# Performance work log

Hardware: AMD Instinct MI355X
Metric: run time of the kernel (lower is better)

Reference implementation:

```python
import jax, jax.numpy as jnp
import numpy as np

N, IN_DIM, H, ATT_DIM, OUT_DIM = 4096, 512, 8, 64, 64
ATT_BIAS = 0.5


def setup_inputs() -> dict:
    key = jax.random.key(0)
    ks = jax.random.split(key, 12)
    s_in = 1.0 / np.sqrt(IN_DIM)
    s_o = 1.0 / np.sqrt(H * OUT_DIM)
    return {
        "Q": jax.random.normal(ks[0], (N, IN_DIM), jnp.float32),
        "K": jax.random.normal(ks[1], (N, IN_DIM), jnp.float32),
        "V": jax.random.normal(ks[2], (N, IN_DIM), jnp.float32),
        "adj": jax.random.uniform(ks[3], (N, N), jnp.float32),
        "WQ": jax.random.normal(ks[4], (IN_DIM, H * ATT_DIM), jnp.float32) * s_in,
        "bQ": jnp.zeros((H * ATT_DIM,), jnp.float32),
        "WK": jax.random.normal(ks[5], (IN_DIM, H * ATT_DIM), jnp.float32) * s_in,
        "bK": jnp.zeros((H * ATT_DIM,), jnp.float32),
        "WV": jax.random.normal(ks[6], (IN_DIM, H * OUT_DIM), jnp.float32) * s_in,
        "bV": jnp.zeros((H * OUT_DIM,), jnp.float32),
        "WO": jax.random.normal(ks[7], (H * OUT_DIM, OUT_DIM), jnp.float32) * s_o,
        "bO": jnp.zeros((OUT_DIM,), jnp.float32),
    }


def reference(Q, K, V, adj, WQ, bQ, WK, bK, WV, bV, WO, bO):
    scale = ATT_DIM ** -0.5
    q = (Q @ WQ + bQ).reshape(N, H, ATT_DIM)   # [N,H,d]
    k = (K @ WK + bK).reshape(N, H, ATT_DIM)   # [N,H,d]
    v = (V @ WV + bV).reshape(N, H, OUT_DIM)   # [N,H,e]
    # scaled QK^T per head: [H,N,N]
    scores = jnp.einsum("nhd,mhd->hnm", q * scale, k)
    # sigmoid -> bias subtract -> +0.1*adj -> softmax over keys
    scores = jax.nn.sigmoid(scores) - ATT_BIAS + 0.1 * adj[None, :, :]
    attn = jax.nn.softmax(scores, axis=2)
    # attend values (dropout p=0 => identity), concat heads, project
    out = jnp.einsum("hnm,mhe->nhe", attn, v).reshape(N, H * OUT_DIM)
    return out @ WO + bO
```

## Files before the change

kernel.cpp:

```cpp
#include <hip/hip_runtime.h>
#include <hip/hip_bf16.h>

#define N_TOK  4096
#define HD     512
#define NH     8
#define NSPLIT 2

typedef short v8s __attribute__((ext_vector_type(8)));
typedef float v4f __attribute__((ext_vector_type(4)));
typedef unsigned short u16;

#define QSCALE   0.18033688011112042f
#define ADJ2     0.14426950408889634f
#define EA0 0.999410f
#define EA1 1.016220f
#define EA2 0.423120f
#define EA3 0.279120f

__device__ __forceinline__ float bf2f(u16 x) {
  union { unsigned int u; float f; } c; c.u = ((unsigned int)x) << 16; return c.f;
}
__device__ __forceinline__ u16 f2bf(float f) {
  union { float f; unsigned int u; } c; c.f = f;
  return (u16)((c.u + 0x7fffu + ((c.u >> 16) & 1u)) >> 16);
}
__device__ __forceinline__ float fast_exp2(float x) {
#if __has_builtin(__builtin_amdgcn_exp2f)
  return __builtin_amdgcn_exp2f(x);
#else
  return exp2f(x);
#endif
}
__device__ __forceinline__ unsigned int pk_bf16(float a, float b) {
  union { __hip_bfloat162 h; unsigned int u; } c;
  c.h = __float22bfloat162_rn(make_float2(a, b));
  return c.u;
}

__device__ __forceinline__ bool detect_f32(const u16* __restrict__ q) {
  int l = threadIdx.x & 63;
  u16 e = q[2 * l];
  float x = bf2f(e);
  int ex = (e >> 7) & 0xFF;
  float ax = fabsf(x);
  bool ok = (ex != 0xFF) && (ax < 64.f) && (ax > 1e-30f);
  unsigned long long m = __ballot(ok);
  return __popcll(m) < 48;
}
__device__ __forceinline__ float bias_ld(const void* b, int i, bool f32) {
  return f32 ? ((const float*)b)[i] : bf2f(((const u16*)b)[i]);
}

__global__ __launch_bounds__(256) void conv_adjE_k(const void* __restrict__ adj, u16* __restrict__ adjE,
                                                   const u16* __restrict__ Qdet) {
  bool f32 = detect_f32(Qdet);
  int i = blockIdx.x * 256 + threadIdx.x;
  float4 f;
  if (f32) {
    f = ((const float4*)adj)[i];
  } else {
    short4 v = ((const short4*)adj)[i];
    f.x = bf2f((u16)v.x); f.y = bf2f((u16)v.y); f.z = bf2f((u16)v.z); f.w = bf2f((u16)v.w);
  }
  unsigned int d0 = pk_bf16(fast_exp2(f.x * ADJ2), fast_exp2(f.y * ADJ2));
  unsigned int d1 = pk_bf16(fast_exp2(f.z * ADJ2), fast_exp2(f.w * ADJ2));
  ((uint2*)adjE)[i] = make_uint2(d0, d1);
}

__global__ __launch_bounds__(256) void tr_w_k(const void* W0, const void* W1, const void* W2, const void* W3,
                                              u16* t0, u16* t1, u16* t2, u16* t3,
                                              const u16* __restrict__ Qdet) {
  bool f32 = detect_f32(Qdet);
  int z = blockIdx.z;
  const void* in; u16* out; int C;
  if (z == 0)      { in = W0; out = t0; C = 512; }
  else if (z == 1) { in = W1; out = t1; C = 512; }
  else if (z == 2) { in = W2; out = t2; C = 512; }
  else             { in = W3; out = t3; C = 64; if (blockIdx.y) return; }
  const int R = 512;
  __shared__ __align__(16) u16 tile[64][72];
  const int r0 = blockIdx.x * 64, c0 = blockIdx.y * 64;
  const int t = threadIdx.x;
#pragma unroll
  for (int rep = 0; rep < 2; ++rep) {
    int idx = (t + rep * 256) * 8;
    int r = idx >> 6, c = idx & 63;
    if (f32) {
      const float* sp = (const float*)in + (size_t)(r0 + r) * C + (c0 + c);
      float4 a = *(const float4*)sp, b = *(const float4*)(sp + 4);
      uint4 q = make_uint4(pk_bf16(a.x, a.y), pk_bf16(a.z, a.w),
                           pk_bf16(b.x, b.y), pk_bf16(b.z, b.w));
      *(uint4*)&tile[r][c] = q;
    } else {
      *(v8s*)&tile[r][c] = *(const v8s*)((const u16*)in + (size_t)(r0 + r) * C + (c0 + c));
    }
  }
  __syncthreads();
#pragma unroll
  for (int rep = 0; rep < 2; ++rep) {
    int idx = (t + rep * 256) * 8;
    int oc = idx >> 6, orr = idx & 63;
    u16 tmp[8];
#pragma unroll
    for (int j = 0; j < 8; ++j) tmp[j] = tile[orr + j][oc];
    *(v8s*)(out + (size_t)(c0 + oc) * R + (r0 + orr)) = *(v8s*)tmp;
  }
}

__global__ __launch_bounds__(256) void gemm_qkv_k(const void* A0, const void* A1, const void* A2,
                                                  const u16* __restrict__ t0, const u16* __restrict__ t1,
                                                  const u16* __restrict__ t2,
                                                  const void* b0, const void* b1, const void* b2,
                                                  u16* __restrict__ qb, u16* __restrict__ kb,
                                                  u16* __restrict__ vtb) {
  __shared__ __align__(16) u16 As[64][72];
  __shared__ __align__(16) u16 Bs[64][72];
  bool f32 = detect_f32((const u16*)A0);
  int z = blockIdx.z;
  const void* Araw = (z == 0) ? A0 : (z == 1) ? A1 : A2;
  const u16* Bt    = (z == 0) ? t0 : (z == 1) ? t1 : t2;
  const void* bias = (z == 0) ? b0 : (z == 1) ? b1 : b2;
  const bool vt = (z == 2);
  const int i0 = blockIdx.x * 64, j0 = blockIdx.y * 64;
  const int t = threadIdx.x, w = t >> 6, l = t & 63, quad = l >> 4, l15 = l & 15;
  v4f acc[4] = {};
  for (int k0 = 0; k0 < 512; k0 += 64) {
#pragma unroll
    for (int rep = 0; rep < 2; ++rep) {
      int idx = (t + rep * 256) * 8;
      int r = idx >> 6, c = idx & 63;
      if (f32) {
        const float* sp = (const float*)Araw + (size_t)(i0 + r) * 512 + k0 + c;
        float4 fa = *(const float4*)sp, fb = *(const float4*)(sp + 4);
        uint4 q = make_uint4(pk_bf16(fa.x, fa.y), pk_bf16(fa.z, fa.w),
                             pk_bf16(fb.x, fb.y), pk_bf16(fb.z, fb.w));
        *(uint4*)&As[r][c] = q;
      } else {
        *(v8s*)&As[r][c] = *(const v8s*)((const u16*)Araw + (size_t)(i0 + r) * 512 + k0 + c);
      }
      *(v8s*)&Bs[r][c] = *(const v8s*)(Bt + (size_t)(j0 + r) * 512 + k0 + c);
    }
    __syncthreads();
    if (vt) {
#pragma unroll
      for (int h = 0; h < 2; ++h) {
        v8s a = *(const v8s*)&As[w * 16 + l15][h * 32 + quad * 8];
#pragma unroll
        for (int cb = 0; cb < 4; ++cb) {
          v8s b = *(const v8s*)&Bs[cb * 16 + l15][h * 32 + quad * 8];
          acc[cb] = __builtin_amdgcn_mfma_f32_16x16x32_bf16(b, a, acc[cb], 0, 0, 0);
        }
      }
    } else {
#pragma unroll
      for (int h = 0; h < 2; ++h) {
        v8s a = *(const v8s*)&As[w * 16 + l15][h * 32 + quad * 8];
#pragma unroll
        for (int cb = 0; cb < 4; ++cb) {
          v8s b = *(const v8s*)&Bs[cb * 16 + l15][h * 32 + quad * 8];
          acc[cb] = __builtin_amdgcn_mfma_f32_16x16x32_bf16(a, b, acc[cb], 0, 0, 0);
        }
      }
    }
    __syncthreads();
  }
  if (vt) {
#pragma unroll
    for (int cb = 0; cb < 4; ++cb) {
#pragma unroll
      for (int r = 0; r < 4; ++r) {
        int jj = j0 + cb * 16 + quad * 4 + r;
        int ii = i0 + w * 16 + l15;
        vtb[(size_t)jj * N_TOK + ii] = f2bf(acc[cb][r] + bias_ld(bias, jj, f32));
      }
    }
  } else {
    const float oscale = (z == 0) ? QSCALE : 1.0f;
    u16* C = (z == 0) ? qb : kb;
#pragma unroll
    for (int cb = 0; cb < 4; ++cb) {
      int col = j0 + cb * 16 + l15;
      float bv = bias_ld(bias, col, f32);
#pragma unroll
      for (int r = 0; r < 4; ++r) {
        int row = i0 + w * 16 + quad * 4 + r;
        C[(size_t)row * HD + col] = f2bf((acc[cb][r] + bv) * oscale);
      }
    }
  }
}

__global__ __launch_bounds__(256, 4) void attn_kernel(const u16* __restrict__ qb, const u16* __restrict__ kb,
                                                      const u16* __restrict__ vtb, const u16* __restrict__ adjE,
                                                      u16* __restrict__ Opart, float* __restrict__ Lpart) {
  __shared__ __align__(16) u16 Ks[64][72];
  __shared__ __align__(16) u16 Vs[64][72];
  __shared__ __align__(16) u16 Ps[4][16][72];
  const int i0 = blockIdx.x * 64, h64 = blockIdx.y * 64, z = blockIdx.z;
  const int t = threadIdx.x, w = t >> 6, l = t & 63, quad = l >> 4, l15 = l & 15;
  const int iRow = i0 + w * 16 + l15;

  v8s qf[2];
#pragma unroll
  for (int h = 0; h < 2; ++h)
    qf[h] = *(const v8s*)(qb + (size_t)iRow * HD + h64 + h * 32 + quad * 8);

  const u16* adjRow = adjE + (size_t)iRow * N_TOK;
  v4f oacc[4] = {};
  float lsum = 0.f;

  const int m_begin = z * (N_TOK / NSPLIT);
  for (int m0 = m_begin; m0 < m_begin + N_TOK / NSPLIT; m0 += 64) {
    uint2 av[4];
#pragma unroll
    for (int cb = 0; cb < 4; ++cb)
      av[cb] = *(const uint2*)(adjRow + m0 + cb * 16 + quad * 4);

#pragma unroll
    for (int rep = 0; rep < 2; ++rep) {
      int idx = (t + rep * 256) * 8;
      int r = idx >> 6, c = idx & 63;
      *(v8s*)&Ks[r][c] = *(const v8s*)(kb  + (size_t)(m0 + r) * HD + h64 + c);
      *(v8s*)&Vs[r][c] = *(const v8s*)(vtb + (size_t)(h64 + r) * N_TOK + m0 + c);
    }
    __syncthreads();

    v4f s[4] = {};
#pragma unroll
    for (int h = 0; h < 2; ++h) {
#pragma unroll
      for (int cb = 0; cb < 4; ++cb) {
        v8s kf = *(const v8s*)&Ks[cb * 16 + l15][h * 32 + quad * 8];
        s[cb] = __builtin_amdgcn_mfma_f32_16x16x32_bf16(kf, qf[h], s[cb], 0, 0, 0);
      }
    }

#pragma unroll
    for (int cb = 0; cb < 4; ++cb) {
      union { unsigned int u; float f; } e0, e1, e2, e3;
      e0.u = av[cb].x << 16; e1.u = av[cb].x & 0xFFFF0000u;
      e2.u = av[cb].y << 16; e3.u = av[cb].y & 0xFFFF0000u;
      float r0 = __builtin_amdgcn_rcpf(1.f + fast_exp2(-s[cb][0]));
      float r1 = __builtin_amdgcn_rcpf(1.f + fast_exp2(-s[cb][1]));
      float r2 = __builtin_amdgcn_rcpf(1.f + fast_exp2(-s[cb][2]));
      float r3 = __builtin_amdgcn_rcpf(1.f + fast_exp2(-s[cb][3]));
      float p0 = e0.f * fmaf(fmaf(fmaf(EA3, r0, EA2), r0, EA1), r0, EA0);
      float p1 = e1.f * fmaf(fmaf(fmaf(EA3, r1, EA2), r1, EA1), r1, EA0);
      float p2 = e2.f * fmaf(fmaf(fmaf(EA3, r2, EA2), r2, EA1), r2, EA0);
      float p3 = e3.f * fmaf(fmaf(fmaf(EA3, r3, EA2), r3, EA1), r3, EA0);
      lsum += (p0 + p1) + (p2 + p3);
      *(uint2*)&Ps[w][l15][cb * 16 + quad * 4] = make_uint2(pk_bf16(p0, p1), pk_bf16(p2, p3));
    }
    asm volatile("s_waitcnt lgkmcnt(0)" ::: "memory");

#pragma unroll
    for (int h = 0; h < 2; ++h) {
      v8s pa = *(const v8s*)&Ps[w][l15][h * 32 + quad * 8];
#pragma unroll
      for (int eb = 0; eb < 4; ++eb) {
        v8s vf = *(const v8s*)&Vs[eb * 16 + l15][h * 32 + quad * 8];
        oacc[eb] = __builtin_amdgcn_mfma_f32_16x16x32_bf16(pa, vf, oacc[eb], 0, 0, 0);
      }
    }
    __syncthreads();
  }

  lsum += __shfl_xor(lsum, 16);
  lsum += __shfl_xor(lsum, 32);
  if (l < 16)
    Lpart[((size_t)z * N_TOK + i0 + w * 16 + l) * NH + blockIdx.y] = lsum;
#pragma unroll
  for (int eb = 0; eb < 4; ++eb) {
#pragma unroll
    for (int r = 0; r < 4; ++r) {
      size_t row = (size_t)z * N_TOK + i0 + w * 16 + quad * 4 + r;
      Opart[row * HD + h64 + eb * 16 + l15] = f2bf(oacc[eb][r]);
    }
  }
}

__global__ __launch_bounds__(256) void gemm_bt(const u16* __restrict__ Opart, const float* __restrict__ Lpart,
                                               const u16* __restrict__ Bt, const void* bias,
                                               void* __restrict__ C, const u16* __restrict__ Qdet) {
  __shared__ __align__(16) u16 As[64][72];
  __shared__ __align__(16) u16 Bs[64][72];
  bool f32 = detect_f32(Qdet);
  const int i0 = blockIdx.x * 64;
  const int t = threadIdx.x, w = t >> 6, l = t & 63, quad = l >> 4, l15 = l & 15;
  v4f acc[4] = {};
  for (int k0 = 0; k0 < 512; k0 += 64) {
    const int h = k0 >> 6;
#pragma unroll
    for (int rep = 0; rep < 2; ++rep) {
      int idx = (t + rep * 256) * 8;
      int r = idx >> 6, c = idx & 63;
      float lv = 0.f;
#pragma unroll
      for (int s = 0; s < NSPLIT; ++s) lv += Lpart[((size_t)s * N_TOK + i0 + r) * NH + h];
      float rl = __builtin_amdgcn_rcpf(lv);
      float vals[8] = {};
#pragma unroll
      for (int s = 0; s < NSPLIT; ++s) {
        v8s ov = *(const v8s*)(Opart + ((size_t)s * N_TOK + i0 + r) * HD + k0 + c);
#pragma unroll
        for (int j = 0; j < 8; ++j) vals[j] += bf2f((u16)ov[j]);
      }
      uint4 q = make_uint4(pk_bf16(vals[0] * rl, vals[1] * rl), pk_bf16(vals[2] * rl, vals[3] * rl),
                           pk_bf16(vals[4] * rl, vals[5] * rl), pk_bf16(vals[6] * rl, vals[7] * rl));
      *(uint4*)&As[r][c] = q;
      *(v8s*)&Bs[r][c] = *(const v8s*)(Bt + (size_t)r * 512 + k0 + c);
    }
    __syncthreads();
#pragma unroll
    for (int h2 = 0; h2 < 2; ++h2) {
      v8s a = *(const v8s*)&As[w * 16 + l15][h2 * 32 + quad * 8];
#pragma unroll
      for (int cb = 0; cb < 4; ++cb) {
        v8s b = *(const v8s*)&Bs[cb * 16 + l15][h2 * 32 + quad * 8];
        acc[cb] = __builtin_amdgcn_mfma_f32_16x16x32_bf16(a, b, acc[cb], 0, 0, 0);
      }
    }
    __syncthreads();
  }
#pragma unroll
  for (int cb = 0; cb < 4; ++cb) {
    int col = cb * 16 + l15;
    float bv = bias_ld(bias, col, f32);
#pragma unroll
    for (int r = 0; r < 4; ++r) {
      int row = i0 + w * 16 + quad * 4 + r;
      float v = acc[cb][r] + bv;
      size_t idx = (size_t)row * 64 + col;
      if (f32) ((float*)C)[idx] = v;
      else     ((u16*)C)[idx] = f2bf(v);
    }
  }
}

extern "C" void kernel_launch(void* const* d_in, const int* in_sizes, int n_in,
                              void* d_out, int out_size, void* d_ws, size_t ws_size,
                              hipStream_t stream) {
  (void)in_sizes; (void)n_in; (void)out_size; (void)ws_size;
  const void* Q   = d_in[0];
  const void* K   = d_in[1];
  const void* V   = d_in[2];
  const void* adj = d_in[3];
  const void* WQ  = d_in[4];
  const void* bQ  = d_in[5];
  const void* WK  = d_in[6];
  const void* bK  = d_in[7];
  const void* WV  = d_in[8];
  const void* bV  = d_in[9];
  const void* WO  = d_in[10];
  const void* bO  = d_in[11];
  const u16* Qdet = (const u16*)Q;

  char* p = (char*)d_ws;
  auto alloc = [&](size_t bytes) { char* r = p; p += (bytes + 255) & ~(size_t)255; return r; };
  const size_t SZ = (size_t)N_TOK * HD * 2;

  u16* adjE    = (u16*)alloc((size_t)N_TOK * N_TOK * 2);
  u16* qb      = (u16*)alloc(SZ);
  u16* kb      = (u16*)alloc(SZ);
  u16* vtb     = (u16*)alloc(SZ);
  u16* Opart   = (u16*)alloc((size_t)NSPLIT * SZ);
  float* Lpart = (float*)alloc((size_t)NSPLIT * N_TOK * NH * 4);
  u16* tQ      = (u16*)alloc((size_t)512 * 512 * 2);
  u16* tK      = (u16*)alloc((size_t)512 * 512 * 2);
  u16* tV      = (u16*)alloc((size_t)512 * 512 * 2);
  u16* tO      = (u16*)alloc((size_t)64 * 512 * 2);

  dim3 b256(256);
  conv_adjE_k<<<dim3(16384), b256, 0, stream>>>(adj, adjE, Qdet);
  tr_w_k<<<dim3(8, 8, 4), b256, 0, stream>>>(WQ, WK, WV, WO, tQ, tK, tV, tO, Qdet);
  gemm_qkv_k<<<dim3(64, 8, 3), b256, 0, stream>>>(Q, K, V, tQ, tK, tV,
                                                  bQ, bK, bV, qb, kb, vtb);
  attn_kernel<<<dim3(N_TOK / 64, NH, NSPLIT), b256, 0, stream>>>(qb, kb, vtb, adjE, Opart, Lpart);
  gemm_bt<<<dim3(64, 1), b256, 0, stream>>>(Opart, Lpart, tO, bO, d_out, Qdet);
}
```

Measured before the change: 269.4 us.

## Restructure attention kernel with 32x32 MFMA, register-resident P, double-buffered async loads

The attention kernel now processes 128 query rows per block with 32x32x16 bf16 MFMAs. The P tile stays in registers and is rearranged with v_permlane32_swap instead of being staged through LDS. K and V tiles are double-buffered in XOR-swizzled LDS and filled with global_load_lds, so the next tile loads while the current one computes. The key range is also split four ways instead of two, to keep the grid large. This is meant to cut LDS traffic, bank conflicts and load latency stalls, at the cost of more registers (two 16-float accumulators plus the P fragments), possible occupancy limits, and more partial results for the final reduction.

```diff
diff --git a/kernel.cpp b/kernel.cpp
--- a/kernel.cpp
+++ b/kernel.cpp
@@ -4,10 +4,13 @@
 #define N_TOK  4096
 #define HD     512
 #define NH     8
-#define NSPLIT 2
+#define NSPLIT 4
+#define QBLK   128
+#define NT     ((N_TOK / NSPLIT) / 64)
 
 typedef short v8s __attribute__((ext_vector_type(8)));
 typedef float v4f __attribute__((ext_vector_type(4)));
+typedef float v16f __attribute__((ext_vector_type(16)));
 typedef unsigned short u16;
 
 #define QSCALE   0.18033688011112042f
@@ -35,6 +38,15 @@
   union { __hip_bfloat162 h; unsigned int u; } c;
   c.h = __float22bfloat162_rn(make_float2(a, b));
   return c.u;
+}
+
+typedef __attribute__((address_space(1))) const char gchar;
+typedef __attribute__((address_space(3))) char lchar;
+__device__ __forceinline__ void glds16(const void* g, void* l) {
+  __builtin_amdgcn_global_load_lds((gchar*)g, (lchar*)l, 16, 0, 0);
+}
+__device__ __forceinline__ void plswap(unsigned int& a, unsigned int& b) {
+  asm volatile("v_permlane32_swap_b32 %0, %1" : "+v"(a), "+v"(b));
 }
 
 __device__ __forceinline__ bool detect_f32(const u16* __restrict__ q) {
@@ -193,89 +205,124 @@
 __global__ __launch_bounds__(256, 4) void attn_kernel(const u16* __restrict__ qb, const u16* __restrict__ kb,
                                                       const u16* __restrict__ vtb, const u16* __restrict__ adjE,
                                                       u16* __restrict__ Opart, float* __restrict__ Lpart) {
-  __shared__ __align__(16) u16 Ks[64][72];
-  __shared__ __align__(16) u16 Vs[64][72];
-  __shared__ __align__(16) u16 Ps[4][16][72];
-  const int i0 = blockIdx.x * 64, h64 = blockIdx.y * 64, z = blockIdx.z;
-  const int t = threadIdx.x, w = t >> 6, l = t & 63, quad = l >> 4, l15 = l & 15;
-  const int iRow = i0 + w * 16 + l15;
-
-  v8s qf[2];
-#pragma unroll
-  for (int h = 0; h < 2; ++h)
-    qf[h] = *(const v8s*)(qb + (size_t)iRow * HD + h64 + h * 32 + quad * 8);
-
-  const u16* adjRow = adjE + (size_t)iRow * N_TOK;
-  v4f oacc[4] = {};
+  __shared__ __align__(16) u16 Ks[2][64 * 64];
+  __shared__ __align__(16) u16 Vs[2][64 * 64];
+  const int i0 = blockIdx.x * QBLK, h64 = blockIdx.y * 64, z = blockIdx.z;
+  const int t = threadIdx.x, w = t >> 6, l = t & 63;
+  const int il = l & 31, h2 = l >> 5, il7 = il & 7;
+  const int iRow = i0 + w * 32 + il;
+
+  v8s qf[4];
+#pragma unroll
+  for (int c = 0; c < 4; ++c)
+    qf[c] = *(const v8s*)(qb + (size_t)iRow * HD + h64 + 16 * c + 8 * h2);
+
+  const u16* adjRow = adjE + (size_t)iRow * N_TOK + 4 * h2;
+
+  const int srow = l >> 3;
+  const int scol = ((l & 7) ^ srow) * 8;
+  const int ldsrow = 16 * w;
+
+  v16f oacc0 = {}, oacc1 = {};
   float lsum = 0.f;
-
   const int m_begin = z * (N_TOK / NSPLIT);
-  for (int m0 = m_begin; m0 < m_begin + N_TOK / NSPLIT; m0 += 64) {
-    uint2 av[4];
-#pragma unroll
-    for (int cb = 0; cb < 4; ++cb)
-      av[cb] = *(const uint2*)(adjRow + m0 + cb * 16 + quad * 4);
-
-#pragma unroll
-    for (int rep = 0; rep < 2; ++rep) {
-      int idx = (t + rep * 256) * 8;
-      int r = idx >> 6, c = idx & 63;
-      *(v8s*)&Ks[r][c] = *(const v8s*)(kb  + (size_t)(m0 + r) * HD + h64 + c);
-      *(v8s*)&Vs[r][c] = *(const v8s*)(vtb + (size_t)(h64 + r) * N_TOK + m0 + c);
+
+#pragma unroll
+  for (int n = 0; n < 2; ++n) {
+    int r = ldsrow + 8 * n + srow;
+    glds16(kb + (size_t)(m_begin + r) * HD + h64 + scol, &Ks[0][(ldsrow + 8 * n) * 64]);
+    glds16(vtb + (size_t)(h64 + r) * N_TOK + m_begin + scol, &Vs[0][(ldsrow + 8 * n) * 64]);
+  }
+  __syncthreads();
+
+  int buf = 0;
+  for (int mt = 0; mt < NT; ++mt) {
+    const int m0 = m_begin + mt * 64;
+    if (mt + 1 < NT) {
+      const int m1 = m0 + 64;
+#pragma unroll
+      for (int n = 0; n < 2; ++n) {
+        int r = ldsrow + 8 * n + srow;
+        glds16(kb + (size_t)(m1 + r) * HD + h64 + scol, &Ks[buf ^ 1][(ldsrow + 8 * n) * 64]);
+        glds16(vtb + (size_t)(h64 + r) * N_TOK + m1 + scol, &Vs[buf ^ 1][(ldsrow + 8 * n) * 64]);
+      }
+    }
+    const u16* Kb = &Ks[buf][0];
+    const u16* Vb = &Vs[buf][0];
+
+#pragma unroll
+    for (int mh = 0; mh < 2; ++mh) {
+      uint2 av[4];
+#pragma unroll
+      for (int rq = 0; rq < 4; ++rq)
+        av[rq] = *(const uint2*)(adjRow + m0 + 32 * mh + 8 * rq);
+
+      v16f macc = {};
+      __builtin_amdgcn_s_setprio(1);
+#pragma unroll
+      for (int c = 0; c < 4; ++c) {
+        v8s kf = *(const v8s*)(Kb + (32 * mh + il) * 64 + (((2 * c + h2) ^ il7) * 8));
+        macc = __builtin_amdgcn_mfma_f32_32x32x16_bf16(kf, qf[c], macc, 0, 0, 0);
+      }
+      __builtin_amdgcn_s_setprio(0);
+
+      float p[16];
+#pragma unroll
+      for (int rq = 0; rq < 4; ++rq) {
+        union { unsigned int u; float f; } e0, e1, e2, e3;
+        e0.u = av[rq].x << 16; e1.u = av[rq].x & 0xFFFF0000u;
+        e2.u = av[rq].y << 16; e3.u = av[rq].y & 0xFFFF0000u;
+        float r0 = __builtin_amdgcn_rcpf(1.f + fast_exp2(-macc[4 * rq + 0]));
+        float r1 = __builtin_amdgcn_rcpf(1.f + fast_exp2(-macc[4 * rq + 1]));
+        float r2 = __builtin_amdgcn_rcpf(1.f + fast_exp2(-macc[4 * rq + 2]));
+        float r3 = __builtin_amdgcn_rcpf(1.f + fast_exp2(-macc[4 * rq + 3]));
+        float p0 = e0.f * fmaf(fmaf(fmaf(EA3, r0, EA2), r0, EA1), r0, EA0);
+        float p1 = e1.f * fmaf(fmaf(fmaf(EA3, r1, EA2), r1, EA1), r1, EA0);
+        float p2 = e2.f * fmaf(fmaf(fmaf(EA3, r2, EA2), r2, EA1), r2, EA0);
+        float p3 = e3.f * fmaf(fmaf(fmaf(EA3, r3, EA2), r3, EA1), r3, EA0);
+        lsum += (p0 + p1) + (p2 + p3);
+        p[4 * rq + 0] = p0; p[4 * rq + 1] = p1; p[4 * rq + 2] = p2; p[4 * rq + 3] = p3;
+      }
+
+      v8s pf[2];
+#pragma unroll
+      for (int sub = 0; sub < 2; ++sub) {
+        unsigned int u0 = pk_bf16(p[8 * sub + 0], p[8 * sub + 1]);
+        unsigned int u1 = pk_bf16(p[8 * sub + 2], p[8 * sub + 3]);
+        unsigned int u2 = pk_bf16(p[8 * sub + 4], p[8 * sub + 5]);
+        unsigned int u3 = pk_bf16(p[8 * sub + 6], p[8 * sub + 7]);
+        plswap(u0, u2); plswap(u1, u3);
+        union { uint4 q; v8s v; } pu;
+        pu.q = make_uint4(u0, u1, u2, u3);
+        pf[sub] = pu.v;
+      }
+
+      __builtin_amdgcn_s_setprio(1);
+#pragma unroll
+      for (int sub = 0; sub < 2; ++sub) {
+        const int mc = 2 * mh + sub;
+        v8s vf0 = *(const v8s*)(Vb + (il) * 64      + (((2 * mc + h2) ^ il7) * 8));
+        v8s vf1 = *(const v8s*)(Vb + (32 + il) * 64 + (((2 * mc + h2) ^ il7) * 8));
+        oacc0 = __builtin_amdgcn_mfma_f32_32x32x16_bf16(pf[sub], vf0, oacc0, 0, 0, 0);
+        oacc1 = __builtin_amdgcn_mfma_f32_32x32x16_bf16(pf[sub], vf1, oacc1, 0, 0, 0);
+      }
+      __builtin_amdgcn_s_setprio(0);
     }
     __syncthreads();
-
-    v4f s[4] = {};
-#pragma unroll
-    for (int h = 0; h < 2; ++h) {
-#pragma unroll
-      for (int cb = 0; cb < 4; ++cb) {
-        v8s kf = *(const v8s*)&Ks[cb * 16 + l15][h * 32 + quad * 8];
-        s[cb] = __builtin_amdgcn_mfma_f32_16x16x32_bf16(kf, qf[h], s[cb], 0, 0, 0);
-      }
-    }
-
-#pragma unroll
-    for (int cb = 0; cb < 4; ++cb) {
-      union { unsigned int u; float f; } e0, e1, e2, e3;
-      e0.u = av[cb].x << 16; e1.u = av[cb].x & 0xFFFF0000u;
-      e2.u = av[cb].y << 16; e3.u = av[cb].y & 0xFFFF0000u;
-      float r0 = __builtin_amdgcn_rcpf(1.f + fast_exp2(-s[cb][0]));
-      float r1 = __builtin_amdgcn_rcpf(1.f + fast_exp2(-s[cb][1]));
-      float r2 = __builtin_amdgcn_rcpf(1.f + fast_exp2(-s[cb][2]));
-      float r3 = __builtin_amdgcn_rcpf(1.f + fast_exp2(-s[cb][3]));
-      float p0 = e0.f * fmaf(fmaf(fmaf(EA3, r0, EA2), r0, EA1), r0, EA0);
-      float p1 = e1.f * fmaf(fmaf(fmaf(EA3, r1, EA2), r1, EA1), r1, EA0);
-      float p2 = e2.f * fmaf(fmaf(fmaf(EA3, r2, EA2), r2, EA1), r2, EA0);
-      float p3 = e3.f * fmaf(fmaf(fmaf(EA3, r3, EA2), r3, EA1), r3, EA0);
-      lsum += (p0 + p1) + (p2 + p3);
-      *(uint2*)&Ps[w][l15][cb * 16 + quad * 4] = make_uint2(pk_bf16(p0, p1), pk_bf16(p2, p3));
-    }
-    asm volatile("s_waitcnt lgkmcnt(0)" ::: "memory");
-
-#pragma unroll
-    for (int h = 0; h < 2; ++h) {
-      v8s pa = *(const v8s*)&Ps[w][l15][h * 32 + quad * 8];
-#pragma unroll
-      for (int eb = 0; eb < 4; ++eb) {
-        v8s vf = *(const v8s*)&Vs[eb * 16 + l15][h * 32 + quad * 8];
-        oacc[eb] = __builtin_amdgcn_mfma_f32_16x16x32_bf16(pa, vf, oacc[eb], 0, 0, 0);
-      }
-    }
-    __syncthreads();
-  }
-
-  lsum += __shfl_xor(lsum, 16);
+    buf ^= 1;
+  }
+
   lsum += __shfl_xor(lsum, 32);
-  if (l < 16)
-    Lpart[((size_t)z * N_TOK + i0 + w * 16 + l) * NH + blockIdx.y] = lsum;
-#pragma unroll
-  for (int eb = 0; eb < 4; ++eb) {
-#pragma unroll
-    for (int r = 0; r < 4; ++r) {
-      size_t row = (size_t)z * N_TOK + i0 + w * 16 + quad * 4 + r;
-      Opart[row * HD + h64 + eb * 16 + l15] = f2bf(oacc[eb][r]);
-    }
+  if (l < 32)
+    Lpart[((size_t)z * N_TOK + i0 + 32 * w + il) * NH + blockIdx.y] = lsum;
+
+#pragma unroll
+  for (int r = 0; r < 16; ++r) {
+    int i_local = (r & 3) + 8 * (r >> 2) + 4 * h2;
+    size_t row = (size_t)z * N_TOK + i0 + 32 * w + i_local;
+    u16* op = Opart + row * HD + h64 + il;
+    op[0]  = f2bf(oacc0[r]);
+    op[32] = f2bf(oacc1[r]);
   }
 }
 
@@ -375,6 +422,6 @@
   tr_w_k<<<dim3(8, 8, 4), b256, 0, stream>>>(WQ, WK, WV, WO, tQ, tK, tV, tO, Qdet);
   gemm_qkv_k<<<dim3(64, 8, 3), b256, 0, stream>>>(Q, K, V, tQ, tK, tV,
                                                   bQ, bK, bV, qb, kb, vtb);
-  attn_kernel<<<dim3(N_TOK / 64, NH, NSPLIT), b256, 0, stream>>>(qb, kb, vtb, adjE, Opart, Lpart);
+  attn_kernel<<<dim3(N_TOK / QBLK, NH, NSPLIT), b256, 0, stream>>>(qb, kb, vtb, adjE, Opart, Lpart);
   gemm_bt<<<dim3(64, 1), b256, 0, stream>>>(Opart, Lpart, tO, bO, d_out, Qdet);
 }
```

Measured after the change: 263.9 us. -2.1%, faster.
